# Kernel tuning notes

Measured on AMD Instinct MI355X. Metric: run time of the kernel, lower is better.

The kernel has to match this reference:

```python
import jax, jax.numpy as jnp
import numpy as np

N = 100000      # nodes
E = 1600000     # edges
G = 64          # graphs in batch
F_IN = 128
HID = 16        # per-head hidden of conv1
H = 8           # heads of conv1
F_OUT = 16
NEG_SLOPE = 0.2


def setup_inputs() -> dict:
    key = jax.random.key(0)
    ks = jax.random.split(key, 11)
    x = jax.random.normal(ks[0], (N, F_IN), jnp.float32)
    edge_index = jax.random.randint(ks[1], (2, E), 0, N, jnp.int32)
    batch = jnp.sort(jax.random.randint(ks[2], (N,), 0, G, jnp.int32))
    s_in = 1.0 / np.sqrt(F_IN)
    s_h = 1.0 / np.sqrt(HID)
    s_mid = 1.0 / np.sqrt(H * HID)
    W1 = jax.random.normal(ks[3], (F_IN, H * HID), jnp.float32) * s_in
    att1_src = jax.random.normal(ks[4], (H, HID), jnp.float32) * s_h
    att1_dst = jax.random.normal(ks[5], (H, HID), jnp.float32) * s_h
    b1 = jnp.zeros((H * HID,), jnp.float32)
    W2 = jax.random.normal(ks[6], (H * HID, F_OUT), jnp.float32) * s_mid
    att2_src = jax.random.normal(ks[7], (1, F_OUT), jnp.float32) * (1.0 / np.sqrt(F_OUT))
    att2_dst = jax.random.normal(ks[8], (1, F_OUT), jnp.float32) * (1.0 / np.sqrt(F_OUT))
    b2 = jnp.zeros((F_OUT,), jnp.float32)
    return {"x": x, "edge_index": edge_index, "batch": batch,
            "W1": W1, "att1_src": att1_src, "att1_dst": att1_dst, "b1": b1,
            "W2": W2, "att2_src": att2_src, "att2_dst": att2_dst, "b2": b2}


def _gat_conv(x, edge_index, W, a_src, a_dst, b, concat):
    """PyG GATConv: h = xW; e_ij = leaky_relu(a_src.h_j + a_dst.h_i);
    softmax over in-edges of each dst node i; out_i = sum_j alpha_ij h_j."""
    src, dst = edge_index[0], edge_index[1]
    n = x.shape[0]
    nh, c = a_src.shape
    h = (x @ W).reshape(n, nh, c)                      # [N,H,C]
    a_s = jnp.einsum('nhc,hc->nh', h, a_src)           # [N,H]
    a_d = jnp.einsum('nhc,hc->nh', h, a_dst)
    e = jax.nn.leaky_relu(a_s[src] + a_d[dst], NEG_SLOPE)   # [E,H]
    m = jax.lax.stop_gradient(jax.ops.segment_max(e, dst, num_segments=n))
    ex = jnp.exp(e - m[dst])
    denom = jax.ops.segment_sum(ex, dst, num_segments=n)
    alpha = ex / (denom[dst] + 1e-16)                  # [E,H]
    msg = h[src] * alpha[:, :, None]                   # [E,H,C]
    out = jax.ops.segment_sum(msg, dst, num_segments=n)  # [N,H,C]
    out = out.reshape(n, nh * c) if concat else out.mean(axis=1)
    return out + b


def reference(x, edge_index, batch, W1, att1_src, att1_dst, b1,
              W2, att2_src, att2_dst, b2):
    h = _gat_conv(x, edge_index, W1, att1_src, att1_dst, b1, concat=True)
    h = jax.nn.elu(h)
    # F.dropout(p=0.6, training=False) -> identity in eval mode
    h = _gat_conv(h, edge_index, W2, att2_src, att2_dst, b2, concat=False)
    counts = jax.ops.segment_sum(jnp.ones((h.shape[0],), h.dtype), batch, num_segments=G)
    pooled = jax.ops.segment_sum(h, batch, num_segments=G) / jnp.maximum(counts, 1.0)[:, None]
    return jax.nn.log_softmax(pooled, axis=1)
```

## Files before the change

kernel.cpp:

```cpp
#include <hip/hip_runtime.h>
#include <cstdint>
#include <cstddef>

typedef unsigned short ushort_t;
typedef unsigned int uint_t;
typedef __attribute__((ext_vector_type(8))) short bf16x8;
typedef __attribute__((ext_vector_type(4))) float f32x4;

#define NBMAX 1024
#define EPB   16384
#define LDK   136

__device__ inline ushort_t f2bf(float f) {
  uint_t u = __float_as_uint(f);
  uint_t r = (u + 0x7fffu + ((u >> 16) & 1u)) >> 16;
  return (ushort_t)r;
}
__device__ inline float bfl(uint_t u) { return __uint_as_float(u << 16); }
__device__ inline float bfh(uint_t u) { return __uint_as_float(u & 0xffff0000u); }
__device__ inline float bf1(ushort_t v) { return __uint_as_float(((uint_t)v) << 16); }


__global__ void bucket_hist_kernel(const int* __restrict__ edst, int* __restrict__ gcount,
                                   int* __restrict__ myBase, int E, int NB) {
  __shared__ int hist[NBMAX];
  int t = threadIdx.x;
  int blk = blockIdx.x;
  for (int i = t; i < NB; i += 256) hist[i] = 0;
  __syncthreads();
  int b0 = blk * EPB, e1 = min(b0 + EPB, E);
  for (int i = b0 + t; i < e1; i += 256) atomicAdd(&hist[edst[i] >> 7], 1);
  __syncthreads();
  for (int i = t; i < NB; i += 256) {
    int c = hist[i];
    myBase[(size_t)blk * NB + i] = c ? atomicAdd(&gcount[i], c) : 0;
  }
}

__global__ void bucket_scan_kernel(const int* __restrict__ gcount, int* __restrict__ boff, int NB) {
  __shared__ int ws[16];
  int t = threadIdx.x;
  int lane = t & 63, w = t >> 6;
  int v = (t < NB) ? gcount[t] : 0;
  for (int o = 1; o < 64; o <<= 1) { int y = __shfl_up(v, o); if (lane >= o) v += y; }
  if (lane == 63) ws[w] = v;
  __syncthreads();
  if (t < 16) {
    int s = ws[t];
    for (int o = 1; o < 16; o <<= 1) { int y = __shfl_up(s, o); if (t >= o) s += y; }
    ws[t] = s;
  }
  __syncthreads();
  if (w > 0) v += ws[w - 1];
  if (t < NB) boff[t + 1] = v;
  if (t == 0) boff[0] = 0;
}

__global__ void bucket_scatter_kernel(const int* __restrict__ esrc, const int* __restrict__ edst,
                                      const int* __restrict__ boff, const int* __restrict__ myBase,
                                      uint_t* __restrict__ pairs, int E, int NB) {
  __shared__ int cursor[NBMAX];
  int t = threadIdx.x;
  int blk = blockIdx.x;
  for (int i = t; i < NB; i += 256) cursor[i] = boff[i] + myBase[(size_t)blk * NB + i];
  __syncthreads();
  int b0 = blk * EPB, e1 = min(b0 + EPB, E);
  for (int i = b0 + t; i < e1; i += 256) {
    int d = edst[i], s = esrc[i];
    int pos = atomicAdd(&cursor[d >> 7], 1);
    pairs[pos] = ((uint_t)(d & 127) << 25) | (uint_t)s;
  }
}

__global__ void bucket_csr_kernel(const uint_t* __restrict__ pairs, const int* __restrict__ boff,
                                  int* __restrict__ rowptr, int* __restrict__ csr, int n, int NB) {
  __shared__ int cnt[128];
  __shared__ int ws2[2];
  int b = blockIdx.x;
  int t = threadIdx.x;
  int lo = boff[b], hi = boff[b + 1];
  int D0 = b << 7;
  cnt[t] = 0;
  __syncthreads();
  for (int i = lo + t; i < hi; i += 128) atomicAdd(&cnt[pairs[i] >> 25], 1);
  __syncthreads();
  int lane = t & 63, w = t >> 6;
  int v = cnt[t];
  int vx = v;
  for (int o = 1; o < 64; o <<= 1) { int y = __shfl_up(vx, o); if (lane >= o) vx += y; }
  if (lane == 63) ws2[w] = vx;
  __syncthreads();
  int incl = vx + (w ? ws2[0] : 0);
  int excl = incl - v;
  int d = D0 + t;
  if (d <= n) rowptr[d] = lo + excl;
  __syncthreads();
  cnt[t] = excl;
  __syncthreads();
  for (int i = lo + t; i < hi; i += 128) {
    uint_t pr = pairs[i];
    int pos = atomicAdd(&cnt[pr >> 25], 1);
    csr[lo + pos] = (int)(pr & 0x1FFFFFFu);
  }
}

__global__ void gemm1_att1_kernel(const float* __restrict__ x, const float* __restrict__ W,
                                  const float* __restrict__ asw, const float* __restrict__ adw,
                                  ushort_t* __restrict__ h1b, float* __restrict__ a_s,
                                  float* __restrict__ a_d, int n) {
  __shared__ ushort_t wT[128 * LDK];
  int t = threadIdx.x;
  {
    int nn = t & 127;
    int kp0 = t >> 7;
    for (int kp = kp0; kp < 64; kp += 2) {
      float w0 = W[(size_t)(2 * kp) * 128 + nn];
      float w1 = W[(size_t)(2 * kp + 1) * 128 + nn];
      *(uint_t*)&wT[nn * LDK + 2 * kp] = (uint_t)f2bf(w0) | ((uint_t)f2bf(w1) << 16);
    }
  }
  __syncthreads();

  int lane = t & 63, w = t >> 6;
  int g = lane >> 4, cl = lane & 15;
  int rowA = blockIdx.x * 64 + w * 16 + cl;
  const float* xr = x + (size_t)(rowA < n ? rowA : 0) * 128;

  bf16x8 afr[4];
  #pragma unroll
  for (int c = 0; c < 4; ++c) {
    float4 v0 = *(const float4*)(xr + c * 32 + g * 8);
    float4 v1 = *(const float4*)(xr + c * 32 + g * 8 + 4);
    bf16x8 a;
    a[0] = (short)f2bf(v0.x); a[1] = (short)f2bf(v0.y);
    a[2] = (short)f2bf(v0.z); a[3] = (short)f2bf(v0.w);
    a[4] = (short)f2bf(v1.x); a[5] = (short)f2bf(v1.y);
    a[6] = (short)f2bf(v1.z); a[7] = (short)f2bf(v1.w);
    afr[c] = a;
  }

  int orow0 = blockIdx.x * 64 + w * 16 + g * 4;
  #pragma unroll 2
  for (int tt = 0; tt < 8; ++tt) {
    f32x4 acc = {0.f, 0.f, 0.f, 0.f};
    #pragma unroll
    for (int c = 0; c < 4; ++c) {
      bf16x8 bfr = *(const bf16x8*)&wT[(tt * 16 + cl) * LDK + c * 32 + g * 8];
      acc = __builtin_amdgcn_mfma_f32_16x16x32_bf16(afr[c], bfr, acc, 0, 0, 0);
    }
    float asv = asw[tt * 16 + cl], adv = adw[tt * 16 + cl];
    float ps[4], pd[4];
    ushort_t hb[4];
    #pragma unroll
    for (int r = 0; r < 4; ++r) {
      float v = acc[r];
      hb[r] = f2bf(v);
      ps[r] = v * asv; pd[r] = v * adv;
    }
    #pragma unroll
    for (int o = 1; o < 16; o <<= 1) {
      #pragma unroll
      for (int r = 0; r < 4; ++r) { ps[r] += __shfl_xor(ps[r], o); pd[r] += __shfl_xor(pd[r], o); }
    }
    #pragma unroll
    for (int r = 0; r < 4; ++r) {
      int rr = orow0 + r;
      if (rr < n) {
        h1b[(size_t)rr * 128 + tt * 16 + cl] = hb[r];
        if (cl == 0) {
          a_s[(size_t)rr * 8 + tt] = ps[r];
          a_d[(size_t)rr * 8 + tt] = pd[r];
        }
      }
    }
  }
}

__global__ void alpha1_kernel(const int* __restrict__ rowptr, const int* __restrict__ csr_src,
                              const float* __restrict__ a_s, const float* __restrict__ a_d,
                              ushort_t* __restrict__ alpha1, int n) {
  int t = threadIdx.x & 63;
  int w = threadIdx.x >> 6;
  int dst = blockIdx.x * 4 + w;
  if (dst >= n) return;
  int beg = rowptr[dst], end = rowptr[dst + 1];
  if (beg == end) return;
  int h = t & 7, el = t >> 3;
  float adv = a_d[(size_t)dst * 8 + h];
  float M = -1e30f, S = 0.f;
  for (int base = beg; base < end; base += 8) {
    int eidx = base + el;
    bool valid = eidx < end;
    int s = csr_src[valid ? eidx : beg];
    float e = a_s[(size_t)s * 8 + h] + adv;
    e = e > 0.f ? e : 0.2f * e;
    e = valid ? e : -1e30f;
    float m = e;
    m = fmaxf(m, __shfl_xor(m, 8));
    m = fmaxf(m, __shfl_xor(m, 16));
    m = fmaxf(m, __shfl_xor(m, 32));
    float nm = fmaxf(M, m);
    float p = valid ? __expf(e - nm) : 0.f;
    float ps = p;
    ps += __shfl_xor(ps, 8);
    ps += __shfl_xor(ps, 16);
    ps += __shfl_xor(ps, 32);
    S = S * __expf(M - nm) + ps;
    M = nm;
  }
  float inv = 1.f / (S + 1e-16f);
  for (int base = beg; base < end; base += 8) {
    int eidx = base + el;
    if (eidx < end) {
      int s = csr_src[eidx];
      float e = a_s[(size_t)s * 8 + h] + adv;
      e = e > 0.f ? e : 0.2f * e;
      alpha1[(size_t)eidx * 8 + h] = f2bf(__expf(e - M) * inv);
    }
  }
}

__global__ void gat1_agg_kernel(const int* __restrict__ rowptr, const int* __restrict__ csr_src,
                                const ushort_t* __restrict__ h1b,
                                const ushort_t* __restrict__ alpha1,
                                const float* __restrict__ b1, ushort_t* __restrict__ hmidb, int n) {
  int lane = threadIdx.x & 63;
  int w = threadIdx.x >> 6;
  int dst = blockIdx.x * 4 + w;
  if (dst >= n) return;
  int beg = rowptr[dst], end = rowptr[dst + 1];
  int slot = lane >> 4, c8 = lane & 15;
  int hh = c8 >> 1;
  float acc[8] = {};
  #pragma unroll 2
  for (int e = beg + slot; e < end; e += 4) {
    int si = csr_src[e];
    float a = bf1(alpha1[(size_t)e * 8 + hh]);
    uint4 hv = *(const uint4*)(h1b + (size_t)si * 128 + c8 * 8);
    acc[0] = fmaf(a, bfl(hv.x), acc[0]);
    acc[1] = fmaf(a, bfh(hv.x), acc[1]);
    acc[2] = fmaf(a, bfl(hv.y), acc[2]);
    acc[3] = fmaf(a, bfh(hv.y), acc[3]);
    acc[4] = fmaf(a, bfl(hv.z), acc[4]);
    acc[5] = fmaf(a, bfh(hv.z), acc[5]);
    acc[6] = fmaf(a, bfl(hv.w), acc[6]);
    acc[7] = fmaf(a, bfh(hv.w), acc[7]);
  }
  #pragma unroll
  for (int i = 0; i < 8; ++i) {
    acc[i] += __shfl_xor(acc[i], 16);
    acc[i] += __shfl_xor(acc[i], 32);
  }
  if (slot == 0) {
    ushort_t ob[8];
    #pragma unroll
    for (int i = 0; i < 8; ++i) {
      float v = acc[i] + b1[c8 * 8 + i];
      v = v > 0.f ? v : (__expf(v) - 1.f);
      ob[i] = f2bf(v);
    }
    *(uint4*)(hmidb + (size_t)dst * 128 + c8 * 8) = *(uint4*)ob;
  }
}

__global__ void gemm2_att2_kernel(const ushort_t* __restrict__ hmidb, const float* __restrict__ W2,
                                  const float* __restrict__ asw, const float* __restrict__ adw,
                                  ushort_t* __restrict__ h2b, float* __restrict__ a_s2,
                                  float* __restrict__ a_d2, int n) {
  __shared__ ushort_t wT[16 * LDK];
  int t = threadIdx.x;
  if (t < 128) {
    int nn = t & 15, kp0 = t >> 4;
    for (int kp = kp0; kp < 64; kp += 8) {
      float w0 = W2[(size_t)(2 * kp) * 16 + nn];
      float w1 = W2[(size_t)(2 * kp + 1) * 16 + nn];
      *(uint_t*)&wT[nn * LDK + 2 * kp] = (uint_t)f2bf(w0) | ((uint_t)f2bf(w1) << 16);
    }
  }
  __syncthreads();

  int lane = t & 63, w = t >> 6;
  int g = lane >> 4, cl = lane & 15;
  int rowA = blockIdx.x * 64 + w * 16 + cl;
  const ushort_t* hr = hmidb + (size_t)(rowA < n ? rowA : 0) * 128;

  f32x4 acc = {0.f, 0.f, 0.f, 0.f};
  #pragma unroll
  for (int c = 0; c < 4; ++c) {
    bf16x8 afr = *(const bf16x8*)(hr + c * 32 + g * 8);
    bf16x8 bfr = *(const bf16x8*)&wT[cl * LDK + c * 32 + g * 8];
    acc = __builtin_amdgcn_mfma_f32_16x16x32_bf16(afr, bfr, acc, 0, 0, 0);
  }
  float asv = asw[cl], adv = adw[cl];
  float ps[4], pd[4];
  ushort_t hb[4];
  #pragma unroll
  for (int r = 0; r < 4; ++r) {
    float v = acc[r];
    hb[r] = f2bf(v);
    ps[r] = v * asv; pd[r] = v * adv;
  }
  #pragma unroll
  for (int o = 1; o < 16; o <<= 1) {
    #pragma unroll
    for (int r = 0; r < 4; ++r) { ps[r] += __shfl_xor(ps[r], o); pd[r] += __shfl_xor(pd[r], o); }
  }
  int orow0 = blockIdx.x * 64 + w * 16 + g * 4;
  #pragma unroll
  for (int r = 0; r < 4; ++r) {
    int rr = orow0 + r;
    if (rr < n) {
      h2b[(size_t)rr * 16 + cl] = hb[r];
      if (cl == 0) { a_s2[rr] = ps[r]; a_d2[rr] = pd[r]; }
    }
  }
}

__global__ void alpha2_kernel(const int* __restrict__ rowptr, const int* __restrict__ csr_src,
                              const float* __restrict__ a_s2, const float* __restrict__ a_d2,
                              float* __restrict__ alpha2, int n) {
  int t = threadIdx.x & 63;
  int w = threadIdx.x >> 6;
  int dst = blockIdx.x * 4 + w;
  if (dst >= n) return;
  int beg = rowptr[dst], end = rowptr[dst + 1];
  if (beg == end) return;
  float adv = a_d2[dst];
  float M = -1e30f, S = 0.f;
  for (int base = beg; base < end; base += 64) {
    int eidx = base + t;
    bool valid = eidx < end;
    int s = csr_src[valid ? eidx : beg];
    float e = a_s2[s] + adv;
    e = e > 0.f ? e : 0.2f * e;
    e = valid ? e : -1e30f;
    float m = e;
    #pragma unroll
    for (int o = 1; o < 64; o <<= 1) m = fmaxf(m, __shfl_xor(m, o));
    float nm = fmaxf(M, m);
    float p = valid ? __expf(e - nm) : 0.f;
    float ps = p;
    #pragma unroll
    for (int o = 1; o < 64; o <<= 1) ps += __shfl_xor(ps, o);
    S = S * __expf(M - nm) + ps;
    M = nm;
  }
  float inv = 1.f / (S + 1e-16f);
  for (int base = beg; base < end; base += 64) {
    int eidx = base + t;
    if (eidx < end) {
      int s = csr_src[eidx];
      float e = a_s2[s] + adv;
      e = e > 0.f ? e : 0.2f * e;
      alpha2[eidx] = __expf(e - M) * inv;
    }
  }
}

__global__ void gat2_agg_kernel(const int* __restrict__ rowptr, const int* __restrict__ csr_src,
                                const ushort_t* __restrict__ h2b,
                                const float* __restrict__ alpha2, const float* __restrict__ b2,
                                const int* __restrict__ batch,
                                float* __restrict__ pooled, float* __restrict__ cntb,
                                int n, int G) {
  __shared__ float pooledL[17][16];
  __shared__ float cntL[17];
  int t = threadIdx.x;
  if (t < 17) cntL[t] = 0.f;
  for (int i = t; i < 17 * 16; i += 256) ((float*)pooledL)[i] = 0.f;
  __syncthreads();

  int grp = t >> 4, c = t & 15;
  int dst = blockIdx.x * 16 + grp;
  int gfirst = batch[blockIdx.x * 16];

  if (dst < n) {
    int beg = rowptr[dst], end = rowptr[dst + 1];
    float acc = 0.f;
    for (int base = beg; base < end; base += 16) {
      int cnt = min(16, end - base);
      int idx = min(base + c, end - 1);
      int sv = csr_src[idx];
      float av = alpha2[idx];
      #pragma unroll 4
      for (int i = 0; i < cnt; ++i) {
        float ai = __shfl(av, i, 16);
        int   si = __shfl(sv, i, 16);
        acc = fmaf(ai, bf1(h2b[(size_t)si * 16 + c]), acc);
      }
    }
    float v = acc + b2[c];
    int g = batch[dst];
    int gi = g - gfirst;
    if (gi <= 16) {
      atomicAdd(&pooledL[gi][c], v);
      if (c == 0) atomicAdd(&cntL[gi], 1.f);
    } else {
      atomicAdd(&pooled[g * 16 + c], v);
      if (c == 0) atomicAdd(&cntb[g], 1.f);
    }
  }
  __syncthreads();

  int w = t >> 5, lane32 = t & 31;
  for (int gi = w; gi < 17; gi += 8) {
    if (cntL[gi] > 0.f) {
      int g = gfirst + gi;
      if (lane32 < 16) atomicAdd(&pooled[g * 16 + lane32], pooledL[gi][lane32]);
      else if (lane32 == 16) atomicAdd(&cntb[g], cntL[gi]);
    }
  }
}

__global__ void final_kernel(const float* __restrict__ pooled, const float* __restrict__ cntb,
                             float* __restrict__ out, int G) {
  int g = threadIdx.x;
  if (g >= G) return;
  float c = fmaxf(cntb[g], 1.f);
  float v[16];
  float m = -1e30f;
  #pragma unroll
  for (int i = 0; i < 16; ++i) { v[i] = pooled[g * 16 + i] / c; m = fmaxf(m, v[i]); }
  float s = 0.f;
  #pragma unroll
  for (int i = 0; i < 16; ++i) s += __expf(v[i] - m);
  float ls = logf(s);
  #pragma unroll
  for (int i = 0; i < 16; ++i) out[g * 16 + i] = v[i] - m - ls;
}

extern "C" void kernel_launch(void* const* d_in, const int* in_sizes, int n_in,
                              void* d_out, int out_size, void* d_ws, size_t ws_size,
                              hipStream_t stream) {
  const float* x    = (const float*)d_in[0];
  const int*   eidx = (const int*)  d_in[1];
  const int*   batch= (const int*)  d_in[2];
  const float* W1   = (const float*)d_in[3];
  const float* as1w = (const float*)d_in[4];
  const float* ad1w = (const float*)d_in[5];
  const float* b1   = (const float*)d_in[6];
  const float* W2   = (const float*)d_in[7];
  const float* as2w = (const float*)d_in[8];
  const float* ad2w = (const float*)d_in[9];
  const float* b2   = (const float*)d_in[10];
  float* out = (float*)d_out;

  int N = in_sizes[0] / 128;
  int E = in_sizes[1] / 2;
  int G = out_size / 16;
  const int* esrc = eidx;
  const int* edst = eidx + E;

  int NB = (N + 127) >> 7;
  int nblkA = (E + EPB - 1) / EPB;

  char* p = (char*)d_ws;
  auto alloc = [&](size_t bytes) {
    char* r = p;
    p += (bytes + 255) & ~(size_t)255;
    return r;
  };
  ushort_t* h1b = (ushort_t*)alloc((size_t)N * 128 * 2);
  ushort_t* hmidb = (ushort_t*)alloc((size_t)N * 128 * 2);
  ushort_t* h2b = (ushort_t*)alloc((size_t)N * 16 * 2);
  float* as1  = (float*)alloc((size_t)N * 8 * 4);
  float* ad1  = (float*)alloc((size_t)N * 8 * 4);
  float* as2  = (float*)alloc((size_t)N * 4);
  float* ad2  = (float*)alloc((size_t)N * 4);
  size_t a1sz = (size_t)E * 8 * 2, a2sz = (size_t)E * 4;
  size_t unionSz = a1sz + a2sz;
  char* U = alloc(unionSz);
  uint_t* pairs = (uint_t*)U;
  ushort_t* alpha1 = (ushort_t*)U;
  float* alpha2 = (float*)(U + a1sz);
  float* pooled = (float*)alloc((size_t)(G * 16 + G) * 4);
  float* cntb = pooled + G * 16;
  int* rowptr = (int*)alloc((size_t)(N + 1) * 4);
  int* csr    = (int*)alloc((size_t)E * 4);
  int* gcount = (int*)alloc((size_t)(NBMAX + 1) * 4);
  int* boff   = (int*)alloc((size_t)(NBMAX + 1) * 4);
  int* myBase = (int*)alloc((size_t)nblkA * NB * 4);

  hipMemsetAsync(gcount, 0, (size_t)(NBMAX + 1) * 4, stream);
  hipMemsetAsync(pooled, 0, (size_t)(G * 16 + G) * 4, stream);

  bucket_hist_kernel<<<nblkA, 256, 0, stream>>>(edst, gcount, myBase, E, NB);
  bucket_scan_kernel<<<1, 1024, 0, stream>>>(gcount, boff, NB);
  bucket_scatter_kernel<<<nblkA, 256, 0, stream>>>(esrc, edst, boff, myBase, pairs, E, NB);
  bucket_csr_kernel<<<NB, 128, 0, stream>>>(pairs, boff, rowptr, csr, N, NB);

  gemm1_att1_kernel<<<(N + 63) / 64, 256, 0, stream>>>(x, W1, as1w, ad1w, h1b, as1, ad1, N);
  alpha1_kernel<<<(N + 3) / 4, 256, 0, stream>>>(rowptr, csr, as1, ad1, alpha1, N);
  gat1_agg_kernel<<<(N + 3) / 4, 256, 0, stream>>>(rowptr, csr, h1b, alpha1, b1, hmidb, N);
  gemm2_att2_kernel<<<(N + 63) / 64, 256, 0, stream>>>(hmidb, W2, as2w, ad2w, h2b, as2, ad2, N);
  alpha2_kernel<<<(N + 3) / 4, 256, 0, stream>>>(rowptr, csr, as2, ad2, alpha2, N);
  gat2_agg_kernel<<<(N + 15) / 16, 256, 0, stream>>>(rowptr, csr, h2b, alpha2, b2, batch, pooled, cntb, N, G);
  final_kernel<<<1, (G + 63) / 64 * 64, 0, stream>>>(pooled, cntb, out, G);
}
```

Before: 426.0 us.

## Reuse W tile across row tiles, cache edge scores, and single-pass small-degree softmax

gemm1 now processes two 64-row tiles per block, so the bf16 transpose of W1 into LDS is paid once per 128 rows instead of once per 64. alpha1 keeps the leaky-relu edge scores in LDS for nodes with degree up to 64, avoiding a second gather of csr_src and a_s in the normalisation pass. alpha2 handles degree up to 64 in one pass with a single max and sum reduction. gat2_agg stages the source indices and alphas in LDS instead of broadcasting them by shuffle, and always runs 16 iterations, so short rows pay for padded zero-weight gathers.

```diff
diff --git a/kernel.cpp b/kernel.cpp
--- a/kernel.cpp
+++ b/kernel.cpp
@@ -123,53 +123,57 @@
 
   int lane = t & 63, w = t >> 6;
   int g = lane >> 4, cl = lane & 15;
-  int rowA = blockIdx.x * 64 + w * 16 + cl;
-  const float* xr = x + (size_t)(rowA < n ? rowA : 0) * 128;
-
-  bf16x8 afr[4];
-  #pragma unroll
-  for (int c = 0; c < 4; ++c) {
-    float4 v0 = *(const float4*)(xr + c * 32 + g * 8);
-    float4 v1 = *(const float4*)(xr + c * 32 + g * 8 + 4);
-    bf16x8 a;
-    a[0] = (short)f2bf(v0.x); a[1] = (short)f2bf(v0.y);
-    a[2] = (short)f2bf(v0.z); a[3] = (short)f2bf(v0.w);
-    a[4] = (short)f2bf(v1.x); a[5] = (short)f2bf(v1.y);
-    a[6] = (short)f2bf(v1.z); a[7] = (short)f2bf(v1.w);
-    afr[c] = a;
-  }
-
-  int orow0 = blockIdx.x * 64 + w * 16 + g * 4;
-  #pragma unroll 2
-  for (int tt = 0; tt < 8; ++tt) {
-    f32x4 acc = {0.f, 0.f, 0.f, 0.f};
+
+  #pragma unroll
+  for (int rt = 0; rt < 2; ++rt) {
+    int rowA = blockIdx.x * 128 + rt * 64 + w * 16 + cl;
+    const float* xr = x + (size_t)(rowA < n ? rowA : 0) * 128;
+
+    bf16x8 afr[4];
     #pragma unroll
     for (int c = 0; c < 4; ++c) {
-      bf16x8 bfr = *(const bf16x8*)&wT[(tt * 16 + cl) * LDK + c * 32 + g * 8];
-      acc = __builtin_amdgcn_mfma_f32_16x16x32_bf16(afr[c], bfr, acc, 0, 0, 0);
-    }
-    float asv = asw[tt * 16 + cl], adv = adw[tt * 16 + cl];
-    float ps[4], pd[4];
-    ushort_t hb[4];
-    #pragma unroll
-    for (int r = 0; r < 4; ++r) {
-      float v = acc[r];
-      hb[r] = f2bf(v);
-      ps[r] = v * asv; pd[r] = v * adv;
-    }
-    #pragma unroll
-    for (int o = 1; o < 16; o <<= 1) {
+      float4 v0 = *(const float4*)(xr + c * 32 + g * 8);
+      float4 v1 = *(const float4*)(xr + c * 32 + g * 8 + 4);
+      bf16x8 a;
+      a[0] = (short)f2bf(v0.x); a[1] = (short)f2bf(v0.y);
+      a[2] = (short)f2bf(v0.z); a[3] = (short)f2bf(v0.w);
+      a[4] = (short)f2bf(v1.x); a[5] = (short)f2bf(v1.y);
+      a[6] = (short)f2bf(v1.z); a[7] = (short)f2bf(v1.w);
+      afr[c] = a;
+    }
+
+    int orow0 = blockIdx.x * 128 + rt * 64 + w * 16 + g * 4;
+    #pragma unroll 2
+    for (int tt = 0; tt < 8; ++tt) {
+      f32x4 acc = {0.f, 0.f, 0.f, 0.f};
       #pragma unroll
-      for (int r = 0; r < 4; ++r) { ps[r] += __shfl_xor(ps[r], o); pd[r] += __shfl_xor(pd[r], o); }
-    }
-    #pragma unroll
-    for (int r = 0; r < 4; ++r) {
-      int rr = orow0 + r;
-      if (rr < n) {
-        h1b[(size_t)rr * 128 + tt * 16 + cl] = hb[r];
-        if (cl == 0) {
-          a_s[(size_t)rr * 8 + tt] = ps[r];
-          a_d[(size_t)rr * 8 + tt] = pd[r];
+      for (int c = 0; c < 4; ++c) {
+        bf16x8 bfr = *(const bf16x8*)&wT[(tt * 16 + cl) * LDK + c * 32 + g * 8];
+        acc = __builtin_amdgcn_mfma_f32_16x16x32_bf16(afr[c], bfr, acc, 0, 0, 0);
+      }
+      float asv = asw[tt * 16 + cl], adv = adw[tt * 16 + cl];
+      float ps[4], pd[4];
+      ushort_t hb[4];
+      #pragma unroll
+      for (int r = 0; r < 4; ++r) {
+        float v = acc[r];
+        hb[r] = f2bf(v);
+        ps[r] = v * asv; pd[r] = v * adv;
+      }
+      #pragma unroll
+      for (int o = 1; o < 16; o <<= 1) {
+        #pragma unroll
+        for (int r = 0; r < 4; ++r) { ps[r] += __shfl_xor(ps[r], o); pd[r] += __shfl_xor(pd[r], o); }
+      }
+      #pragma unroll
+      for (int r = 0; r < 4; ++r) {
+        int rr = orow0 + r;
+        if (rr < n) {
+          h1b[(size_t)rr * 128 + tt * 16 + cl] = hb[r];
+          if (cl == 0) {
+            a_s[(size_t)rr * 8 + tt] = ps[r];
+            a_d[(size_t)rr * 8 + tt] = pd[r];
+          }
         }
       }
     }
@@ -179,43 +183,79 @@
 __global__ void alpha1_kernel(const int* __restrict__ rowptr, const int* __restrict__ csr_src,
                               const float* __restrict__ a_s, const float* __restrict__ a_d,
                               ushort_t* __restrict__ alpha1, int n) {
+  __shared__ float e_lds[4][64][8];
   int t = threadIdx.x & 63;
   int w = threadIdx.x >> 6;
   int dst = blockIdx.x * 4 + w;
   if (dst >= n) return;
   int beg = rowptr[dst], end = rowptr[dst + 1];
-  if (beg == end) return;
+  int deg = end - beg;
+  if (deg == 0) return;
   int h = t & 7, el = t >> 3;
   float adv = a_d[(size_t)dst * 8 + h];
   float M = -1e30f, S = 0.f;
-  for (int base = beg; base < end; base += 8) {
-    int eidx = base + el;
-    bool valid = eidx < end;
-    int s = csr_src[valid ? eidx : beg];
-    float e = a_s[(size_t)s * 8 + h] + adv;
-    e = e > 0.f ? e : 0.2f * e;
-    e = valid ? e : -1e30f;
-    float m = e;
-    m = fmaxf(m, __shfl_xor(m, 8));
-    m = fmaxf(m, __shfl_xor(m, 16));
-    m = fmaxf(m, __shfl_xor(m, 32));
-    float nm = fmaxf(M, m);
-    float p = valid ? __expf(e - nm) : 0.f;
-    float ps = p;
-    ps += __shfl_xor(ps, 8);
-    ps += __shfl_xor(ps, 16);
-    ps += __shfl_xor(ps, 32);
-    S = S * __expf(M - nm) + ps;
-    M = nm;
-  }
-  float inv = 1.f / (S + 1e-16f);
-  for (int base = beg; base < end; base += 8) {
-    int eidx = base + el;
-    if (eidx < end) {
-      int s = csr_src[eidx];
+
+  if (deg <= 64) {
+    int nch = (deg + 7) >> 3;
+    for (int it = 0; it < nch; ++it) {
+      int eidx = beg + it * 8 + el;
+      bool valid = eidx < end;
+      int s = csr_src[valid ? eidx : beg];
+      float eraw = a_s[(size_t)s * 8 + h] + adv;
+      eraw = eraw > 0.f ? eraw : 0.2f * eraw;
+      e_lds[w][it * 8 + el][h] = eraw;
+      float e = valid ? eraw : -1e30f;
+      float m = e;
+      m = fmaxf(m, __shfl_xor(m, 8));
+      m = fmaxf(m, __shfl_xor(m, 16));
+      m = fmaxf(m, __shfl_xor(m, 32));
+      float nm = fmaxf(M, m);
+      float p = valid ? __expf(e - nm) : 0.f;
+      float ps = p;
+      ps += __shfl_xor(ps, 8);
+      ps += __shfl_xor(ps, 16);
+      ps += __shfl_xor(ps, 32);
+      S = S * __expf(M - nm) + ps;
+      M = nm;
+    }
+    float inv = 1.f / (S + 1e-16f);
+    for (int it = 0; it < nch; ++it) {
+      int eidx = beg + it * 8 + el;
+      if (eidx < end) {
+        float e = e_lds[w][it * 8 + el][h];
+        alpha1[(size_t)eidx * 8 + h] = f2bf(__expf(e - M) * inv);
+      }
+    }
+  } else {
+    for (int base = beg; base < end; base += 8) {
+      int eidx = base + el;
+      bool valid = eidx < end;
+      int s = csr_src[valid ? eidx : beg];
       float e = a_s[(size_t)s * 8 + h] + adv;
       e = e > 0.f ? e : 0.2f * e;
-      alpha1[(size_t)eidx * 8 + h] = f2bf(__expf(e - M) * inv);
+      e = valid ? e : -1e30f;
+      float m = e;
+      m = fmaxf(m, __shfl_xor(m, 8));
+      m = fmaxf(m, __shfl_xor(m, 16));
+      m = fmaxf(m, __shfl_xor(m, 32));
+      float nm = fmaxf(M, m);
+      float p = valid ? __expf(e - nm) : 0.f;
+      float ps = p;
+      ps += __shfl_xor(ps, 8);
+      ps += __shfl_xor(ps, 16);
+      ps += __shfl_xor(ps, 32);
+      S = S * __expf(M - nm) + ps;
+      M = nm;
+    }
+    float inv = 1.f / (S + 1e-16f);
+    for (int base = beg; base < end; base += 8) {
+      int eidx = base + el;
+      if (eidx < end) {
+        int s = csr_src[eidx];
+        float e = a_s[(size_t)s * 8 + h] + adv;
+        e = e > 0.f ? e : 0.2f * e;
+        alpha1[(size_t)eidx * 8 + h] = f2bf(__expf(e - M) * inv);
+      }
     }
   }
 }
@@ -324,8 +364,28 @@
   int dst = blockIdx.x * 4 + w;
   if (dst >= n) return;
   int beg = rowptr[dst], end = rowptr[dst + 1];
-  if (beg == end) return;
+  int deg = end - beg;
+  if (deg == 0) return;
   float adv = a_d2[dst];
+
+  if (deg <= 64) {
+    int eidx = beg + t;
+    bool valid = eidx < end;
+    int s = csr_src[valid ? eidx : beg];
+    float e = a_s2[s] + adv;
+    e = e > 0.f ? e : 0.2f * e;
+    float ev = valid ? e : -1e30f;
+    float m = ev;
+    #pragma unroll
+    for (int o = 1; o < 64; o <<= 1) m = fmaxf(m, __shfl_xor(m, o));
+    float p = valid ? __expf(ev - m) : 0.f;
+    float S = p;
+    #pragma unroll
+    for (int o = 1; o < 64; o <<= 1) S += __shfl_xor(S, o);
+    if (valid) alpha2[eidx] = p / (S + 1e-16f);
+    return;
+  }
+
   float M = -1e30f, S = 0.f;
   for (int base = beg; base < end; base += 64) {
     int eidx = base + t;
@@ -365,6 +425,8 @@
                                 int n, int G) {
   __shared__ float pooledL[17][16];
   __shared__ float cntL[17];
+  __shared__ int   s_lds[16][16];
+  __shared__ float a_lds[16][16];
   int t = threadIdx.x;
   if (t < 17) cntL[t] = 0.f;
   for (int i = t; i < 17 * 16; i += 256) ((float*)pooledL)[i] = 0.f;
@@ -378,15 +440,13 @@
     int beg = rowptr[dst], end = rowptr[dst + 1];
     float acc = 0.f;
     for (int base = beg; base < end; base += 16) {
-      int cnt = min(16, end - base);
-      int idx = min(base + c, end - 1);
-      int sv = csr_src[idx];
-      float av = alpha2[idx];
-      #pragma unroll 4
-      for (int i = 0; i < cnt; ++i) {
-        float ai = __shfl(av, i, 16);
-        int   si = __shfl(sv, i, 16);
-        acc = fmaf(ai, bf1(h2b[(size_t)si * 16 + c]), acc);
+      int idx = base + c;
+      bool v = idx < end;
+      s_lds[grp][c] = v ? csr_src[idx] : 0;
+      a_lds[grp][c] = v ? alpha2[idx] : 0.f;
+      #pragma unroll
+      for (int j = 0; j < 16; ++j) {
+        acc = fmaf(a_lds[grp][j], bf1(h2b[(size_t)s_lds[grp][j] * 16 + c]), acc);
       }
     }
     float v = acc + b2[c];
@@ -489,7 +549,7 @@
   bucket_scatter_kernel<<<nblkA, 256, 0, stream>>>(esrc, edst, boff, myBase, pairs, E, NB);
   bucket_csr_kernel<<<NB, 128, 0, stream>>>(pairs, boff, rowptr, csr, N, NB);
 
-  gemm1_att1_kernel<<<(N + 63) / 64, 256, 0, stream>>>(x, W1, as1w, ad1w, h1b, as1, ad1, N);
+  gemm1_att1_kernel<<<(N + 127) / 128, 256, 0, stream>>>(x, W1, as1w, ad1w, h1b, as1, ad1, N);
   alpha1_kernel<<<(N + 3) / 4, 256, 0, stream>>>(rowptr, csr, as1, ad1, alpha1, N);
   gat1_agg_kernel<<<(N + 3) / 4, 256, 0, stream>>>(rowptr, csr, h1b, alpha1, b1, hmidb, N);
   gemm2_att2_kernel<<<(N + 63) / 64, 256, 0, stream>>>(hmidb, W2, as2w, ad2w, h2b, as2, ad2, N);
```

Result: faster. 404.3 us (-5.1%).
